# Kernel optimization log

Measured on AMD Instinct MI355X. Metric: run time of the kernel, lower is better.

The kernel has to match this reference:

```python
import jax, jax.numpy as jnp
import numpy as np

P = 16          # patch_size
E = 16          # num_experts
K = 4           # top-k
NOISE_STD = 1.0 / E


def setup_inputs() -> dict:
    key = jax.random.key(0)
    k0, k1, k2, k3, k4, k5 = jax.random.split(key, 6)
    B, C, H, W = 8, 128, 512, 512
    FD = 512
    n_patches = (H // P) * (W // P)  # 1024
    x = jax.random.normal(k0, (B, C, H, W), jnp.float32)
    freq_emb = jax.random.normal(k1, (B, FD), jnp.float32)
    # torch does randn_like(logits) * noise_std inside forward; pre-scaled here for determinism
    noise = jax.random.normal(k2, (B, n_patches, E), jnp.float32) * NOISE_STD
    conv_w = jax.random.normal(k3, (E, C, P, P), jnp.float32) * 0.02
    conv_b = jax.random.normal(k4, (E,), jnp.float32) * 0.02
    freq_w = jax.random.normal(k5, (E, FD), jnp.float32) * 0.05
    return {"x": x, "freq_emb": freq_emb, "noise": noise,
            "conv_w": conv_w, "conv_b": conv_b, "freq_w": freq_w}


def reference(x, freq_emb, noise, conv_w, conv_b, freq_w):
    B, C, H, W = x.shape
    h, w = H // P, W // P
    n = h * w
    # patchify conv (kernel=stride=patch_size) == per-patch GEMM
    patches = x.reshape(B, C, h, P, w, P)                      # [B,C,h,P,w,P]
    spatial = jnp.einsum('bchpwq,ecpq->bhwe', patches, conv_w) + conv_b
    spatial = spatial.reshape(B, n, E)                         # b (h w) e
    freq = (freq_emb @ freq_w.T)[:, None, :]                   # [B,1,E]
    logits = spatial + freq                                    # [B,n,E]
    noisy_logits = logits + noise
    gating_scores = jax.nn.softmax(noisy_logits, axis=-1)
    top_k_values, top_k_indices = jax.lax.top_k(gating_scores, K)  # [B,n,K]
    gates = jnp.zeros_like(logits).at[
        jnp.arange(B)[:, None, None],
        jnp.arange(n)[None, :, None],
        top_k_indices,
    ].set(top_k_values)
    aux_loss = jnp.float32(0.0)  # eval path: no importance/load losses
    return gates, top_k_indices, top_k_values, aux_loss
```

## Files before the change

kernel.cpp:

```cpp
#include <hip/hip_runtime.h>

#define B_ 8
#define C_ 128
#define HW_ 512
#define PS 16
#define E_ 16
#define NP 1024
#define FD 512
#define CH_STRIDE (HW_ * HW_)


__global__ void freq_kernel(const float* __restrict__ femb,
                            const float* __restrict__ fw,
                            float* __restrict__ freqf,
                            float* __restrict__ out) {
    int t = threadIdx.x;
    if (t == 0) out[196608] = 0.0f;
    if (t < 128) {
        int b = t >> 4, e = t & 15;
        const float* fe = femb + b * FD;
        const float* w  = fw + e * FD;
        double s = 0.0;
        for (int i = 0; i < FD; ++i)
            s = fma((double)fe[i], (double)w[i], s);
        freqf[t] = (float)s;
    }
}

#define MAC4(XF, WF)                                        \
    acc = __fadd_rn(acc, __fmul_rn((XF).x, (WF).x));        \
    acc = __fadd_rn(acc, __fmul_rn((XF).y, (WF).y));        \
    acc = __fadd_rn(acc, __fmul_rn((XF).z, (WF).z));        \
    acc = __fadd_rn(acc, __fmul_rn((XF).w, (WF).w));

#define GLOAD_LDS(GSRC, LDST)                                                  \
  __builtin_amdgcn_global_load_lds(                                            \
      (const __attribute__((address_space(1))) void*)(GSRC),                   \
      (__attribute__((address_space(3))) void*)(LDST), 16, 0, 0)

#define LROW 260

__global__ __launch_bounds__(256, 2) void patch_route_kernel(
    const float* __restrict__ x,
    const float* __restrict__ noise,
    const float* __restrict__ conv_w,
    const float* __restrict__ conv_b,
    const float* __restrict__ freqf,
    float* __restrict__ out) {

  __shared__ float xs[2][16][LROW];
  __shared__ float ws[2][16][LROW];
  __shared__ float slg[16][16];

  const int blk = blockIdx.x;
  const int b   = blk >> 6;
  const int pg  = blk & 63;
  const int t   = threadIdx.x;
  const int lp  = t >> 4;
  const int e   = t & 15;
  const int lp16 = lp * 16;
  const int patch = pg * 16 + lp;
  const int pi = pg >> 1;
  const int wv   = t >> 6;
  const int lane = t & 63;

  const float* xblk = x + (size_t)b * (C_ * CH_STRIDE)
                        + (size_t)(pi * PS) * HW_ + (pg & 1) * 256;

  {
    const float* xc = xblk;
    const float* wc = conv_w;
    #pragma unroll
    for (int r = 0; r < 4; ++r) {
      const int p = wv * 4 + r;
      GLOAD_LDS(xc + p * HW_ + lane * 4, &xs[0][p][0]);
    }
    #pragma unroll
    for (int r = 0; r < 4; ++r) {
      const int ee = wv * 4 + r;
      GLOAD_LDS(wc + (size_t)ee * 32768 + lane * 4, &ws[0][ee][0]);
    }
  }

  float acc = 0.0f;
  for (int c = 0; c < C_; ++c) {
    const int cur = c & 1;
    if (c + 1 < C_) {
      const int nb = cur ^ 1;
      const float* xc = xblk + (size_t)(c + 1) * CH_STRIDE;
      const float* wc = conv_w + (c + 1) * 256;
      #pragma unroll
      for (int r = 0; r < 4; ++r) {
        const int p = wv * 4 + r;
        GLOAD_LDS(xc + p * HW_ + lane * 4, &xs[nb][p][0]);
      }
      #pragma unroll
      for (int r = 0; r < 4; ++r) {
        const int ee = wv * 4 + r;
        GLOAD_LDS(wc + (size_t)ee * 32768 + lane * 4, &ws[nb][ee][0]);
      }
      asm volatile("s_waitcnt vmcnt(8)" ::: "memory");
    } else {
      asm volatile("s_waitcnt vmcnt(0)" ::: "memory");
    }
    __builtin_amdgcn_s_barrier();
    __builtin_amdgcn_sched_barrier(0);

    #pragma unroll
    for (int p = 0; p < 16; ++p) {
      const float4 x0 = *reinterpret_cast<const float4*>(&xs[cur][p][lp16 +  0]);
      const float4 x1 = *reinterpret_cast<const float4*>(&xs[cur][p][lp16 +  4]);
      const float4 x2 = *reinterpret_cast<const float4*>(&xs[cur][p][lp16 +  8]);
      const float4 x3 = *reinterpret_cast<const float4*>(&xs[cur][p][lp16 + 12]);
      const float4 w0 = *reinterpret_cast<const float4*>(&ws[cur][e][p * 16 +  0]);
      const float4 w1 = *reinterpret_cast<const float4*>(&ws[cur][e][p * 16 +  4]);
      const float4 w2 = *reinterpret_cast<const float4*>(&ws[cur][e][p * 16 +  8]);
      const float4 w3 = *reinterpret_cast<const float4*>(&ws[cur][e][p * 16 + 12]);
      MAC4(x0, w0);
      MAC4(x1, w1);
      MAC4(x2, w2);
      MAC4(x3, w3);
    }

    __builtin_amdgcn_sched_barrier(0);
    __builtin_amdgcn_s_barrier();
  }

  float lg = __fadd_rn(acc, conv_b[e]);
  lg = __fadd_rn(lg, freqf[b * 16 + e]);
  lg = __fadd_rn(lg, noise[((size_t)b * NP + patch) * 16 + e]);

  slg[lp][e] = lg;
  __syncthreads();

  if (t < 16) {
    const int pp = t;
    const int pat = pg * 16 + pp;
    float v[16];
    #pragma unroll
    for (int i = 0; i < 16; ++i) v[i] = slg[pp][i];

    float m = v[0];
    #pragma unroll
    for (int i = 1; i < 16; ++i) m = fmaxf(m, v[i]);

    float ex[16];
    #pragma unroll
    for (int i = 0; i < 16; ++i) ex[i] = expf(v[i] - m);

    float r[8];
    #pragma unroll
    for (int j = 0; j < 8; ++j) r[j] = __fadd_rn(ex[j], ex[j + 8]);
    float d0 = __fadd_rn(__fadd_rn(r[0], r[1]), __fadd_rn(r[2], r[3]));
    float d1 = __fadd_rn(__fadd_rn(r[4], r[5]), __fadd_rn(r[6], r[7]));
    float den = __fadd_rn(d0, d1);

    float s[16];
    #pragma unroll
    for (int i = 0; i < 16; ++i) s[i] = ex[i] / den;

    unsigned mask = 0;
    int bidx[4]; float bval[4];
    #pragma unroll
    for (int j = 0; j < 4; ++j) {
      int bi = 0; float bv = -1.0f;
      #pragma unroll
      for (int i = 0; i < 16; ++i) {
        if (!((mask >> i) & 1u) && s[i] > bv) { bv = s[i]; bi = i; }
      }
      mask |= 1u << bi;
      bidx[j] = bi; bval[j] = bv;
    }

    const size_t po = (size_t)b * NP + pat;
    float* gout = out + po * 16;
    float* iout = out + 131072 + po * 4;
    float* vout = out + 163840 + po * 4;
    #pragma unroll
    for (int j = 0; j < 4; ++j) {
      iout[j] = (float)bidx[j];
      vout[j] = bval[j];
    }
    #pragma unroll
    for (int i = 0; i < 16; ++i)
      gout[i] = ((mask >> i) & 1u) ? s[i] : 0.0f;
  }
}

extern "C" void kernel_launch(void* const* d_in, const int* in_sizes, int n_in,
                              void* d_out, int out_size, void* d_ws, size_t ws_size,
                              hipStream_t stream) {
  const float* x     = (const float*)d_in[0];
  const float* femb  = (const float*)d_in[1];
  const float* noise = (const float*)d_in[2];
  const float* cw    = (const float*)d_in[3];
  const float* cb    = (const float*)d_in[4];
  const float* fw    = (const float*)d_in[5];
  float* out = (float*)d_out;
  float* freqf = (float*)d_ws;

  hipLaunchKernelGGL(freq_kernel, dim3(1), dim3(128), 0, stream,
                     femb, fw, freqf, out);
  hipLaunchKernelGGL(patch_route_kernel, dim3(512), dim3(256), 0, stream,
                     x, noise, cw, cb, freqf, out);
}
```

Baseline: 360.4 us.

## Pre-transpose conv weights and read them from global memory instead of LDS

Adds a small kernel that transposes conv_w into a layout where the 16 experts for each (channel, float4 chunk) sit next to each other. The main kernel then reads weights with coalesced float4 loads from global/L2 instead of staging them through LDS. This drops the weight LDS buffers and their global_load_lds traffic, and removes the padded LROW rows for x. The costs are an extra kernel launch and weight reads in the inner loop that depend on cache latency rather than LDS. Unpadded x rows may also cause LDS bank conflicts.

```diff
diff --git a/kernel.cpp b/kernel.cpp
--- a/kernel.cpp
+++ b/kernel.cpp
@@ -27,6 +27,16 @@
     }
 }
 
+__global__ __launch_bounds__(256) void transpose_w_kernel(
+    const float* __restrict__ cw, float* __restrict__ wT) {
+  const int tid = blockIdx.x * 256 + threadIdx.x;
+  const int e  = tid >> 13;
+  const int c  = (tid >> 6) & 127;
+  const int r4 = tid & 63;
+  const float4 v = reinterpret_cast<const float4*>(cw)[tid];
+  reinterpret_cast<float4*>(wT)[(c * 64 + r4) * 16 + e] = v;
+}
+
 #define MAC4(XF, WF)                                        \
     acc = __fadd_rn(acc, __fmul_rn((XF).x, (WF).x));        \
     acc = __fadd_rn(acc, __fmul_rn((XF).y, (WF).y));        \
@@ -37,8 +47,6 @@
   __builtin_amdgcn_global_load_lds(                                            \
       (const __attribute__((address_space(1))) void*)(GSRC),                   \
       (__attribute__((address_space(3))) void*)(LDST), 16, 0, 0)
-
-#define LROW 260
 
 __global__ __launch_bounds__(256, 2) void patch_route_kernel(
     const float* __restrict__ x,
@@ -46,10 +54,10 @@
     const float* __restrict__ conv_w,
     const float* __restrict__ conv_b,
     const float* __restrict__ freqf,
+    const float* __restrict__ wT,
     float* __restrict__ out) {
 
-  __shared__ float xs[2][16][LROW];
-  __shared__ float ws[2][16][LROW];
+  __shared__ float xs[2][16][256];
   __shared__ float slg[16][16];
 
   const int blk = blockIdx.x;
@@ -64,58 +72,45 @@
   const int wv   = t >> 6;
   const int lane = t & 63;
 
+  const float4* wT4 = reinterpret_cast<const float4*>(wT);
+
   const float* xblk = x + (size_t)b * (C_ * CH_STRIDE)
                         + (size_t)(pi * PS) * HW_ + (pg & 1) * 256;
 
-  {
-    const float* xc = xblk;
-    const float* wc = conv_w;
-    #pragma unroll
-    for (int r = 0; r < 4; ++r) {
-      const int p = wv * 4 + r;
-      GLOAD_LDS(xc + p * HW_ + lane * 4, &xs[0][p][0]);
-    }
-    #pragma unroll
-    for (int r = 0; r < 4; ++r) {
-      const int ee = wv * 4 + r;
-      GLOAD_LDS(wc + (size_t)ee * 32768 + lane * 4, &ws[0][ee][0]);
-    }
+  #pragma unroll
+  for (int r = 0; r < 4; ++r) {
+    const int p = wv * 4 + r;
+    GLOAD_LDS(xblk + p * HW_ + lane * 4, &xs[0][p][0]);
   }
 
   float acc = 0.0f;
   for (int c = 0; c < C_; ++c) {
     const int cur = c & 1;
     if (c + 1 < C_) {
-      const int nb = cur ^ 1;
       const float* xc = xblk + (size_t)(c + 1) * CH_STRIDE;
-      const float* wc = conv_w + (c + 1) * 256;
       #pragma unroll
       for (int r = 0; r < 4; ++r) {
         const int p = wv * 4 + r;
-        GLOAD_LDS(xc + p * HW_ + lane * 4, &xs[nb][p][0]);
+        GLOAD_LDS(xc + p * HW_ + lane * 4, &xs[cur ^ 1][p][0]);
       }
-      #pragma unroll
-      for (int r = 0; r < 4; ++r) {
-        const int ee = wv * 4 + r;
-        GLOAD_LDS(wc + (size_t)ee * 32768 + lane * 4, &ws[nb][ee][0]);
-      }
-      asm volatile("s_waitcnt vmcnt(8)" ::: "memory");
+      asm volatile("s_waitcnt vmcnt(4)" ::: "memory");
     } else {
       asm volatile("s_waitcnt vmcnt(0)" ::: "memory");
     }
     __builtin_amdgcn_s_barrier();
     __builtin_amdgcn_sched_barrier(0);
 
+    const float4* wc = wT4 + c * 1024 + e;
     #pragma unroll
     for (int p = 0; p < 16; ++p) {
       const float4 x0 = *reinterpret_cast<const float4*>(&xs[cur][p][lp16 +  0]);
       const float4 x1 = *reinterpret_cast<const float4*>(&xs[cur][p][lp16 +  4]);
       const float4 x2 = *reinterpret_cast<const float4*>(&xs[cur][p][lp16 +  8]);
       const float4 x3 = *reinterpret_cast<const float4*>(&xs[cur][p][lp16 + 12]);
-      const float4 w0 = *reinterpret_cast<const float4*>(&ws[cur][e][p * 16 +  0]);
-      const float4 w1 = *reinterpret_cast<const float4*>(&ws[cur][e][p * 16 +  4]);
-      const float4 w2 = *reinterpret_cast<const float4*>(&ws[cur][e][p * 16 +  8]);
-      const float4 w3 = *reinterpret_cast<const float4*>(&ws[cur][e][p * 16 + 12]);
+      const float4 w0 = wc[(p * 4 + 0) * 16];
+      const float4 w1 = wc[(p * 4 + 1) * 16];
+      const float4 w2 = wc[(p * 4 + 2) * 16];
+      const float4 w3 = wc[(p * 4 + 3) * 16];
       MAC4(x0, w0);
       MAC4(x1, w1);
       MAC4(x2, w2);
@@ -198,9 +193,12 @@
   const float* fw    = (const float*)d_in[5];
   float* out = (float*)d_out;
   float* freqf = (float*)d_ws;
+  float* wT    = (float*)((char*)d_ws + 1024);
 
   hipLaunchKernelGGL(freq_kernel, dim3(1), dim3(128), 0, stream,
                      femb, fw, freqf, out);
+  hipLaunchKernelGGL(transpose_w_kernel, dim3(512), dim3(256), 0, stream,
+                     cw, wT);
   hipLaunchKernelGGL(patch_route_kernel, dim3(512), dim3(256), 0, stream,
-                     x, noise, cw, cb, freqf, out);
-}
+                     x, noise, cw, cb, freqf, wT, out);
+}
```

New measurement: 1.050 ms. 191% more time.

## Restructure channel loop to single barrier with register double-buffered LDS reads

Applied to the files above, without the earlier changes.

Moves the wait and barrier to the top of each channel iteration, so the next channel's global-to-LDS loads are issued after the barrier and the trailing barrier is removed. Adds register ping-pong buffers so LDS reads for the next patch row overlap the FMA chain of the current one. Lowers launch bounds occupancy hint from 2 to 1 to allow more registers. The full vmcnt(0) wait at the top means less load/compute overlap across channels, and lower occupancy may hurt latency hiding.

```diff
diff --git a/kernel.cpp b/kernel.cpp
--- a/kernel.cpp
+++ b/kernel.cpp
@@ -8,6 +8,7 @@
 #define NP 1024
 #define FD 512
 #define CH_STRIDE (HW_ * HW_)
+#define LROW 260
 
 
 __global__ void freq_kernel(const float* __restrict__ femb,
@@ -38,9 +39,21 @@
       (const __attribute__((address_space(1))) void*)(GSRC),                   \
       (__attribute__((address_space(3))) void*)(LDST), 16, 0, 0)
 
-#define LROW 260
-
-__global__ __launch_bounds__(256, 2) void patch_route_kernel(
+#define LDSLOT(XA, WA, P)                                                      \
+  XA[0] = *reinterpret_cast<const float4*>(xsc + (P) * LROW + lp16 +  0);      \
+  XA[1] = *reinterpret_cast<const float4*>(xsc + (P) * LROW + lp16 +  4);      \
+  XA[2] = *reinterpret_cast<const float4*>(xsc + (P) * LROW + lp16 +  8);      \
+  XA[3] = *reinterpret_cast<const float4*>(xsc + (P) * LROW + lp16 + 12);      \
+  WA[0] = *reinterpret_cast<const float4*>(wsc + (P) * 16 +  0);               \
+  WA[1] = *reinterpret_cast<const float4*>(wsc + (P) * 16 +  4);               \
+  WA[2] = *reinterpret_cast<const float4*>(wsc + (P) * 16 +  8);               \
+  WA[3] = *reinterpret_cast<const float4*>(wsc + (P) * 16 + 12);
+
+#define MACSLOT(XA, WA)                                                        \
+  MAC4(XA[0], WA[0]); MAC4(XA[1], WA[1]);                                      \
+  MAC4(XA[2], WA[2]); MAC4(XA[3], WA[3]);
+
+__global__ __launch_bounds__(256, 1) void patch_route_kernel(
     const float* __restrict__ x,
     const float* __restrict__ noise,
     const float* __restrict__ conv_w,
@@ -67,63 +80,53 @@
   const float* xblk = x + (size_t)b * (C_ * CH_STRIDE)
                         + (size_t)(pi * PS) * HW_ + (pg & 1) * 256;
 
-  {
-    const float* xc = xblk;
-    const float* wc = conv_w;
-    #pragma unroll
-    for (int r = 0; r < 4; ++r) {
-      const int p = wv * 4 + r;
-      GLOAD_LDS(xc + p * HW_ + lane * 4, &xs[0][p][0]);
-    }
-    #pragma unroll
-    for (int r = 0; r < 4; ++r) {
-      const int ee = wv * 4 + r;
-      GLOAD_LDS(wc + (size_t)ee * 32768 + lane * 4, &ws[0][ee][0]);
-    }
+  #pragma unroll
+  for (int r = 0; r < 4; ++r) {
+    const int p = wv * 4 + r;
+    GLOAD_LDS(xblk + p * HW_ + lane * 4, &xs[0][p][0]);
+  }
+  #pragma unroll
+  for (int r = 0; r < 4; ++r) {
+    const int ee = wv * 4 + r;
+    GLOAD_LDS(conv_w + (size_t)ee * 32768 + lane * 4, &ws[0][ee][0]);
   }
 
   float acc = 0.0f;
   for (int c = 0; c < C_; ++c) {
     const int cur = c & 1;
+    asm volatile("s_waitcnt vmcnt(0)" ::: "memory");
+    __builtin_amdgcn_s_barrier();
+    __builtin_amdgcn_sched_barrier(0);
+
     if (c + 1 < C_) {
-      const int nb = cur ^ 1;
       const float* xc = xblk + (size_t)(c + 1) * CH_STRIDE;
       const float* wc = conv_w + (c + 1) * 256;
       #pragma unroll
       for (int r = 0; r < 4; ++r) {
         const int p = wv * 4 + r;
-        GLOAD_LDS(xc + p * HW_ + lane * 4, &xs[nb][p][0]);
+        GLOAD_LDS(xc + p * HW_ + lane * 4, &xs[cur ^ 1][p][0]);
       }
       #pragma unroll
       for (int r = 0; r < 4; ++r) {
         const int ee = wv * 4 + r;
-        GLOAD_LDS(wc + (size_t)ee * 32768 + lane * 4, &ws[nb][ee][0]);
-      }
-      asm volatile("s_waitcnt vmcnt(8)" ::: "memory");
-    } else {
-      asm volatile("s_waitcnt vmcnt(0)" ::: "memory");
-    }
-    __builtin_amdgcn_s_barrier();
-    __builtin_amdgcn_sched_barrier(0);
-
+        GLOAD_LDS(wc + (size_t)ee * 32768 + lane * 4, &ws[cur ^ 1][ee][0]);
+      }
+    }
+
+    const float* xsc = &xs[cur][0][0];
+    const float* wsc = &ws[cur][e][0];
+    float4 xa[4], wa[4], xb[4], wb[4];
+    LDSLOT(xa, wa, 0)
     #pragma unroll
     for (int p = 0; p < 16; ++p) {
-      const float4 x0 = *reinterpret_cast<const float4*>(&xs[cur][p][lp16 +  0]);
-      const float4 x1 = *reinterpret_cast<const float4*>(&xs[cur][p][lp16 +  4]);
-      const float4 x2 = *reinterpret_cast<const float4*>(&xs[cur][p][lp16 +  8]);
-      const float4 x3 = *reinterpret_cast<const float4*>(&xs[cur][p][lp16 + 12]);
-      const float4 w0 = *reinterpret_cast<const float4*>(&ws[cur][e][p * 16 +  0]);
-      const float4 w1 = *reinterpret_cast<const float4*>(&ws[cur][e][p * 16 +  4]);
-      const float4 w2 = *reinterpret_cast<const float4*>(&ws[cur][e][p * 16 +  8]);
-      const float4 w3 = *reinterpret_cast<const float4*>(&ws[cur][e][p * 16 + 12]);
-      MAC4(x0, w0);
-      MAC4(x1, w1);
-      MAC4(x2, w2);
-      MAC4(x3, w3);
-    }
-
-    __builtin_amdgcn_sched_barrier(0);
-    __builtin_amdgcn_s_barrier();
+      if ((p & 1) == 0) {
+        if (p < 15) { LDSLOT(xb, wb, p + 1) }
+        MACSLOT(xa, wa)
+      } else {
+        if (p < 15) { LDSLOT(xa, wa, p + 1) }
+        MACSLOT(xb, wb)
+      }
+    }
   }
 
   float lg = __fadd_rn(acc, conv_b[e]);
```

New measurement: 377.1 us. +4.6%, slower.

## Process a full patch row per block to reuse conv weights across 32 patches

Applied to the files above, without the earlier changes.

Each block now covers a whole row of 32 patches instead of 16, so the 16x256 weight tile staged in LDS is reused for two patch groups and each thread keeps two accumulators. The grid halves to 256 blocks, LDS per block grows, and launch bounds drop to one block per SIMD occupancy hint. This cuts weight-load traffic and LDS weight reads per FMA, but leaves only 256 blocks on a 256-CU part, with less latency hiding.

```diff
diff --git a/kernel.cpp b/kernel.cpp
--- a/kernel.cpp
+++ b/kernel.cpp
@@ -8,6 +8,7 @@
 #define NP 1024
 #define FD 512
 #define CH_STRIDE (HW_ * HW_)
+#define WROW 260
 
 
 __global__ void freq_kernel(const float* __restrict__ femb,
@@ -27,20 +28,18 @@
     }
 }
 
-#define MAC4(XF, WF)                                        \
-    acc = __fadd_rn(acc, __fmul_rn((XF).x, (WF).x));        \
-    acc = __fadd_rn(acc, __fmul_rn((XF).y, (WF).y));        \
-    acc = __fadd_rn(acc, __fmul_rn((XF).z, (WF).z));        \
-    acc = __fadd_rn(acc, __fmul_rn((XF).w, (WF).w));
+#define MAC4(ACC, XF, WF)                                       \
+    ACC = __fadd_rn(ACC, __fmul_rn((XF).x, (WF).x));            \
+    ACC = __fadd_rn(ACC, __fmul_rn((XF).y, (WF).y));            \
+    ACC = __fadd_rn(ACC, __fmul_rn((XF).z, (WF).z));            \
+    ACC = __fadd_rn(ACC, __fmul_rn((XF).w, (WF).w));
 
 #define GLOAD_LDS(GSRC, LDST)                                                  \
   __builtin_amdgcn_global_load_lds(                                            \
       (const __attribute__((address_space(1))) void*)(GSRC),                   \
       (__attribute__((address_space(3))) void*)(LDST), 16, 0, 0)
 
-#define LROW 260
-
-__global__ __launch_bounds__(256, 2) void patch_route_kernel(
+__global__ __launch_bounds__(256, 1) void patch_route_kernel(
     const float* __restrict__ x,
     const float* __restrict__ noise,
     const float* __restrict__ conv_w,
@@ -48,41 +47,36 @@
     const float* __restrict__ freqf,
     float* __restrict__ out) {
 
-  __shared__ float xs[2][16][LROW];
-  __shared__ float ws[2][16][LROW];
-  __shared__ float slg[16][16];
-
-  const int blk = blockIdx.x;
-  const int b   = blk >> 6;
-  const int pg  = blk & 63;
-  const int t   = threadIdx.x;
-  const int lp  = t >> 4;
-  const int e   = t & 15;
+  __shared__ float xs[2][16][512];
+  __shared__ float ws[2][16][WROW];
+  __shared__ float slg[32][16];
+
+  const int blk  = blockIdx.x;
+  const int b    = blk >> 5;
+  const int prow = blk & 31;
+  const int t    = threadIdx.x;
+  const int lp   = t >> 4;
+  const int e    = t & 15;
   const int lp16 = lp * 16;
-  const int patch = pg * 16 + lp;
-  const int pi = pg >> 1;
   const int wv   = t >> 6;
   const int lane = t & 63;
 
   const float* xblk = x + (size_t)b * (C_ * CH_STRIDE)
-                        + (size_t)(pi * PS) * HW_ + (pg & 1) * 256;
-
-  {
-    const float* xc = xblk;
-    const float* wc = conv_w;
-    #pragma unroll
-    for (int r = 0; r < 4; ++r) {
-      const int p = wv * 4 + r;
-      GLOAD_LDS(xc + p * HW_ + lane * 4, &xs[0][p][0]);
-    }
-    #pragma unroll
-    for (int r = 0; r < 4; ++r) {
-      const int ee = wv * 4 + r;
-      GLOAD_LDS(wc + (size_t)ee * 32768 + lane * 4, &ws[0][ee][0]);
-    }
-  }
-
-  float acc = 0.0f;
+                        + (size_t)(prow * PS) * HW_;
+
+  #pragma unroll
+  for (int r = 0; r < 4; ++r) {
+    const int p = wv * 4 + r;
+    GLOAD_LDS(xblk + p * HW_ +       lane * 4, &xs[0][p][0]);
+    GLOAD_LDS(xblk + p * HW_ + 256 + lane * 4, &xs[0][p][256]);
+  }
+  #pragma unroll
+  for (int r = 0; r < 4; ++r) {
+    const int ee = wv * 4 + r;
+    GLOAD_LDS(conv_w + (size_t)ee * 32768 + lane * 4, &ws[0][ee][0]);
+  }
+
+  float acca = 0.0f, accb = 0.0f;
   for (int c = 0; c < C_; ++c) {
     const int cur = c & 1;
     if (c + 1 < C_) {
@@ -92,14 +86,15 @@
       #pragma unroll
       for (int r = 0; r < 4; ++r) {
         const int p = wv * 4 + r;
-        GLOAD_LDS(xc + p * HW_ + lane * 4, &xs[nb][p][0]);
+        GLOAD_LDS(xc + p * HW_ +       lane * 4, &xs[nb][p][0]);
+        GLOAD_LDS(xc + p * HW_ + 256 + lane * 4, &xs[nb][p][256]);
       }
       #pragma unroll
       for (int r = 0; r < 4; ++r) {
         const int ee = wv * 4 + r;
         GLOAD_LDS(wc + (size_t)ee * 32768 + lane * 4, &ws[nb][ee][0]);
       }
-      asm volatile("s_waitcnt vmcnt(8)" ::: "memory");
+      asm volatile("s_waitcnt vmcnt(12)" ::: "memory");
     } else {
       asm volatile("s_waitcnt vmcnt(0)" ::: "memory");
     }
@@ -108,34 +103,46 @@
 
     #pragma unroll
     for (int p = 0; p < 16; ++p) {
-      const float4 x0 = *reinterpret_cast<const float4*>(&xs[cur][p][lp16 +  0]);
-      const float4 x1 = *reinterpret_cast<const float4*>(&xs[cur][p][lp16 +  4]);
-      const float4 x2 = *reinterpret_cast<const float4*>(&xs[cur][p][lp16 +  8]);
-      const float4 x3 = *reinterpret_cast<const float4*>(&xs[cur][p][lp16 + 12]);
-      const float4 w0 = *reinterpret_cast<const float4*>(&ws[cur][e][p * 16 +  0]);
-      const float4 w1 = *reinterpret_cast<const float4*>(&ws[cur][e][p * 16 +  4]);
-      const float4 w2 = *reinterpret_cast<const float4*>(&ws[cur][e][p * 16 +  8]);
-      const float4 w3 = *reinterpret_cast<const float4*>(&ws[cur][e][p * 16 + 12]);
-      MAC4(x0, w0);
-      MAC4(x1, w1);
-      MAC4(x2, w2);
-      MAC4(x3, w3);
+      const float4 xa0 = *reinterpret_cast<const float4*>(&xs[cur][p][lp16 +  0]);
+      const float4 xa1 = *reinterpret_cast<const float4*>(&xs[cur][p][lp16 +  4]);
+      const float4 xa2 = *reinterpret_cast<const float4*>(&xs[cur][p][lp16 +  8]);
+      const float4 xa3 = *reinterpret_cast<const float4*>(&xs[cur][p][lp16 + 12]);
+      const float4 xb0 = *reinterpret_cast<const float4*>(&xs[cur][p][lp16 + 256]);
+      const float4 xb1 = *reinterpret_cast<const float4*>(&xs[cur][p][lp16 + 260]);
+      const float4 xb2 = *reinterpret_cast<const float4*>(&xs[cur][p][lp16 + 264]);
+      const float4 xb3 = *reinterpret_cast<const float4*>(&xs[cur][p][lp16 + 268]);
+      const float4 w0  = *reinterpret_cast<const float4*>(&ws[cur][e][p * 16 +  0]);
+      const float4 w1  = *reinterpret_cast<const float4*>(&ws[cur][e][p * 16 +  4]);
+      const float4 w2  = *reinterpret_cast<const float4*>(&ws[cur][e][p * 16 +  8]);
+      const float4 w3  = *reinterpret_cast<const float4*>(&ws[cur][e][p * 16 + 12]);
+      MAC4(acca, xa0, w0); MAC4(accb, xb0, w0);
+      MAC4(acca, xa1, w1); MAC4(accb, xb1, w1);
+      MAC4(acca, xa2, w2); MAC4(accb, xb2, w2);
+      MAC4(acca, xa3, w3); MAC4(accb, xb3, w3);
     }
 
     __builtin_amdgcn_sched_barrier(0);
     __builtin_amdgcn_s_barrier();
   }
 
-  float lg = __fadd_rn(acc, conv_b[e]);
-  lg = __fadd_rn(lg, freqf[b * 16 + e]);
-  lg = __fadd_rn(lg, noise[((size_t)b * NP + patch) * 16 + e]);
-
-  slg[lp][e] = lg;
+  const int patch_a = prow * 32 + lp;
+  const int patch_b = patch_a + 16;
+  const float cb = conv_b[e];
+  const float fq = freqf[b * 16 + e];
+  float lga = __fadd_rn(acca, cb);
+  lga = __fadd_rn(lga, fq);
+  lga = __fadd_rn(lga, noise[((size_t)b * NP + patch_a) * 16 + e]);
+  float lgb = __fadd_rn(accb, cb);
+  lgb = __fadd_rn(lgb, fq);
+  lgb = __fadd_rn(lgb, noise[((size_t)b * NP + patch_b) * 16 + e]);
+
+  slg[lp][e] = lga;
+  slg[lp + 16][e] = lgb;
   __syncthreads();
 
-  if (t < 16) {
+  if (t < 32) {
     const int pp = t;
-    const int pat = pg * 16 + pp;
+    const int pat = prow * 32 + pp;
     float v[16];
     #pragma unroll
     for (int i = 0; i < 16; ++i) v[i] = slg[pp][i];
@@ -201,6 +208,6 @@
 
   hipLaunchKernelGGL(freq_kernel, dim3(1), dim3(128), 0, stream,
                      femb, fw, freqf, out);
-  hipLaunchKernelGGL(patch_route_kernel, dim3(512), dim3(256), 0, stream,
+  hipLaunchKernelGGL(patch_route_kernel, dim3(256), dim3(256), 0, stream,
                      x, noise, cw, cb, freqf, out);
 }
```

Result: slower. 427.1 us (+18.5%).
